# Performance work log

Measured on AMD Instinct MI355X. Metric: run time of the kernel, lower is better.

The kernel has to match this reference:

```python
import jax, jax.numpy as jnp
import numpy as np

N = 20000   # nodes
E = 160000  # edges
C = 512     # input_size / channels
D = 16      # edge_size
H = 256     # hidden_size
EPS = 1e-5  # BatchNorm eps (eval mode, init running stats: mean=0, var=1)


def setup_inputs() -> dict:
    key = jax.random.key(0)
    ks = jax.random.split(key, 24)
    w = lambda k, shape: (jax.random.normal(k, shape, jnp.float32) * 0.02)
    inp = {
        "x": jax.random.normal(ks[0], (N, C), jnp.float32),
        "edge_index": jax.random.randint(ks[1], (2, E), 0, N, jnp.int32),
        "edge_attr": jax.random.normal(ks[2], (E, D), jnp.float32),
        "goal_feat": jax.random.normal(ks[3], (N, C), jnp.float32),
        # CGConv 1
        "Wf1": w(ks[4], (2 * C + D, C)), "bf1": jnp.zeros((C,), jnp.float32),
        "Ws1": w(ks[5], (2 * C + D, C)), "bs1": jnp.zeros((C,), jnp.float32),
        "g1": jnp.ones((C,), jnp.float32), "be1": jnp.zeros((C,), jnp.float32),
        # CGConv 2
        "Wf2": w(ks[6], (2 * C + D, C)), "bf2": jnp.zeros((C,), jnp.float32),
        "Ws2": w(ks[7], (2 * C + D, C)), "bs2": jnp.zeros((C,), jnp.float32),
        "g2": jnp.ones((C,), jnp.float32), "be2": jnp.zeros((C,), jnp.float32),
        # GCNConv 3, 4
        "W3": w(ks[8], (C, H)), "b3": jnp.zeros((H,), jnp.float32),
        "W4": w(ks[9], (H, H)), "b4": jnp.zeros((H,), jnp.float32),
        # distance MLP: Lin(H+C -> C), ReLU, Lin(C -> 1)
        "Wd1": w(ks[10], (H + C, C)), "bd1": jnp.zeros((C,), jnp.float32),
        "Wd2": w(ks[11], (C, 1)), "bd2": jnp.zeros((1,), jnp.float32),
    }
    return inp


def cg_conv(x, src, dst, edge_attr, Wf, bf, Ws, bs, gamma, beta):
    # PyG CGConv: z = x_i || x_j || e;  m = sigmoid(lin_f(z)) * softplus(lin_s(z))
    # aggr='add' at targets, BatchNorm (eval, init stats), residual.
    z = jnp.concatenate([x[dst], x[src], edge_attr], axis=-1)  # [E, 2C+D]
    m = jax.nn.sigmoid(z @ Wf + bf) * jax.nn.softplus(z @ Ws + bs)  # [E, C]
    agg = jax.ops.segment_sum(m, dst, num_segments=N)  # [N, C]
    agg = agg * (gamma / jnp.sqrt(1.0 + EPS)) + beta   # BN eval (mean=0, var=1)
    return agg + x


def gcn_conv(x, src, dst, W, b):
    # PyG GCNConv with add_self_loops=True, normalize=True
    h = x @ W  # [N, out]
    loop = jnp.arange(N, dtype=src.dtype)
    s = jnp.concatenate([src, loop])
    d = jnp.concatenate([dst, loop])
    deg = jax.ops.segment_sum(jnp.ones_like(d, jnp.float32), d, num_segments=N)
    dinv = jnp.where(deg > 0, jax.lax.rsqrt(jnp.maximum(deg, 1.0)), 0.0)
    norm = dinv[s] * dinv[d]  # [E+N]
    out = jax.ops.segment_sum(norm[:, None] * h[s], d, num_segments=N)
    return out + b


def reference(x, edge_index, edge_attr, goal_feat,
              Wf1, bf1, Ws1, bs1, g1, be1,
              Wf2, bf2, Ws2, bs2, g2, be2,
              W3, b3, W4, b4, Wd1, bd1, Wd2, bd2):
    src = edge_index[0]  # x_j (source)
    dst = edge_index[1]  # x_i (target)
    h = jax.nn.relu(cg_conv(x, src, dst, edge_attr, Wf1, bf1, Ws1, bs1, g1, be1))
    h = jax.nn.relu(cg_conv(h, src, dst, edge_attr, Wf2, bf2, Ws2, bs2, g2, be2))
    h = jax.nn.relu(gcn_conv(h, src, dst, W3, b3))
    h = jax.nn.relu(gcn_conv(h, src, dst, W4, b4))
    z = jnp.concatenate([h, goal_feat], axis=1)  # [N, H+C]
    pred_dist = jax.nn.relu(z @ Wd1 + bd1) @ Wd2 + bd2  # [N, 1]
    return pred_dist, h
```

## Files before the change

### kernel.cpp

```cpp
#include <hip/hip_runtime.h>
#include <stdint.h>

#define NNODES 20000
#define NEDGES 160000
#define NPAD   20096

typedef float f32x4 __attribute__((ext_vector_type(4)));
typedef float f32x2 __attribute__((ext_vector_type(2)));
typedef short s16x8 __attribute__((ext_vector_type(8)));
typedef unsigned int u32x4 __attribute__((ext_vector_type(4)));
typedef _Float16 h16x2 __attribute__((ext_vector_type(2)));

#define L2E 1.44269504088896340736f
#define LN2 0.6931471805599453f

__device__ __forceinline__ float b2f(unsigned short b) {
    unsigned int u = ((unsigned int)b) << 16;
    return __builtin_bit_cast(float, u);
}
__device__ __forceinline__ unsigned short f2b(float f) {
    unsigned int u = __builtin_bit_cast(unsigned int, f);
    unsigned int r = (u + 0x7FFFu + ((u >> 16) & 1u)) >> 16;
    return (unsigned short)r;
}
__device__ __forceinline__ f32x2 unpack2(unsigned int u) {
    f32x2 r;
    r.x = __builtin_bit_cast(float, u << 16);
    r.y = __builtin_bit_cast(float, u & 0xFFFF0000u);
    return r;
}
__device__ __forceinline__ unsigned int packh2(float a, float b) {
    h16x2 h = { (_Float16)a, (_Float16)b };
    return __builtin_bit_cast(unsigned int, h);
}
__device__ __forceinline__ float dot2h(unsigned int a, unsigned int b, float c) {
#if __has_builtin(__builtin_amdgcn_fdot2)
    return __builtin_amdgcn_fdot2(__builtin_bit_cast(h16x2, a),
                                  __builtin_bit_cast(h16x2, b), c, false);
#else
    float d;
    asm("v_dot2_f32_f16 %0, %1, %2, %3" : "=v"(d) : "v"(a), "v"(b), "v"(c));
    return d;
#endif
}
__device__ __forceinline__ float exp2f_fast(float x) {
#if __has_builtin(__builtin_amdgcn_exp2f)
    return __builtin_amdgcn_exp2f(x);
#else
    return __builtin_exp2f(x);
#endif
}
__device__ __forceinline__ float log2f_fast(float x) {
#if __has_builtin(__builtin_amdgcn_logf)
    return __builtin_amdgcn_logf(x);
#else
    return __builtin_log2f(x);
#endif
}

__global__ __launch_bounds__(256) void gemm_bt_kernel(
    const unsigned short* __restrict__ A,
    const unsigned short* __restrict__ BT,
    float* __restrict__ Cf,
    unsigned short* __restrict__ Cb,
    int M, int N, int K,
    const float* __restrict__ bias)
{
    __shared__ unsigned short As[128 * 64];
    __shared__ unsigned short Bs[128 * 64];
    const int tid  = threadIdx.x;
    const int wid  = tid >> 6;
    const int lane = tid & 63;

    const int nwg  = gridDim.x * gridDim.y;
    const int orig = blockIdx.y * gridDim.x + blockIdx.x;
    const int q = nwg >> 3, r = nwg & 7;
    const int xcd = orig & 7;
    const int idx = orig >> 3;
    const int swz = (xcd < r ? xcd * (q + 1) : r * (q + 1) + (xcd - r) * q) + idx;
    const int bm = (swz / gridDim.y) * 128;
    const int bn = (swz % gridDim.y) * 128;

    const int wm = (wid & 1) * 64;
    const int wn = (wid >> 1) * 64;

    f32x4 acc[4][4];
#pragma unroll
    for (int i = 0; i < 4; i++)
#pragma unroll
        for (int j = 0; j < 4; j++) acc[i][j] = {0.f, 0.f, 0.f, 0.f};

    for (int k0 = 0; k0 < K; k0 += 64) {
#pragma unroll
        for (int rr = 0; rr < 4; rr++) {
            int flat = rr * 256 + tid;
            int row  = flat >> 3;
            int part = flat & 7;
            int pg   = part ^ (row & 7);
            const unsigned short* ga = A  + (size_t)(bm + row) * K + k0 + pg * 8;
            const unsigned short* gb = BT + (size_t)(bn + row) * K + k0 + pg * 8;
            __builtin_amdgcn_global_load_lds(
                (const __attribute__((address_space(1))) unsigned int*)ga,
                (__attribute__((address_space(3))) unsigned int*)&As[flat * 8], 16, 0, 0);
            __builtin_amdgcn_global_load_lds(
                (const __attribute__((address_space(1))) unsigned int*)gb,
                (__attribute__((address_space(3))) unsigned int*)&Bs[flat * 8], 16, 0, 0);
        }
        __syncthreads();

        const int kq8 = lane >> 4;
        const int rl  = lane & 15;
#pragma unroll
        for (int kk = 0; kk < 2; kk++) {
            s16x8 af[4], bfr[4];
#pragma unroll
            for (int mi = 0; mi < 4; mi++) {
                int row = wm + mi * 16 + rl;
                int slot = (kk * 4 + kq8) ^ (row & 7);
                af[mi] = *(const s16x8*)&As[row * 64 + slot * 8];
            }
#pragma unroll
            for (int ni = 0; ni < 4; ni++) {
                int row = wn + ni * 16 + rl;
                int slot = (kk * 4 + kq8) ^ (row & 7);
                bfr[ni] = *(const s16x8*)&Bs[row * 64 + slot * 8];
            }
#pragma unroll
            for (int mi = 0; mi < 4; mi++)
#pragma unroll
                for (int ni = 0; ni < 4; ni++)
                    acc[mi][ni] = __builtin_amdgcn_mfma_f32_16x16x32_bf16(
                        af[mi], bfr[ni], acc[mi][ni], 0, 0, 0);
        }
        __syncthreads();
    }

    const int cl = lane & 15;
    const int rq = (lane >> 4) * 4;
#pragma unroll
    for (int mi = 0; mi < 4; mi++)
#pragma unroll
        for (int ni = 0; ni < 4; ni++)
#pragma unroll
            for (int rr = 0; rr < 4; rr++) {
                int row = bm + wm + mi * 16 + rq + rr;
                int col = bn + wn + ni * 16 + cl;
                float v = acc[mi][ni][rr];
                if (Cb) {
                    if (bias) v = fmaxf(v + bias[col], 0.f);
                    Cb[(size_t)row * N + col] = f2b(v);
                } else {
                    Cf[(size_t)row * N + col] = v;
                }
            }
}

__global__ void count_kernel(const int* __restrict__ ei, int* __restrict__ counts) {
    int e = blockIdx.x * blockDim.x + threadIdx.x;
    if (e < NEDGES) atomicAdd(&counts[ei[NEDGES + e]], 1);
}

__global__ __launch_bounds__(1024) void scan_kernel(const int* __restrict__ counts,
                                                    int* __restrict__ row_ptr)
{
    __shared__ int sdata[1024];
    const int t = threadIdx.x;
    int vals[20];
    const int base = t * 20;
    int lsum = 0;
#pragma unroll
    for (int j = 0; j < 20; j++) {
        int idx = base + j;
        int v = (idx < NNODES) ? counts[idx] : 0;
        vals[j] = v; lsum += v;
    }
    sdata[t] = lsum;
    __syncthreads();
    for (int off = 1; off < 1024; off <<= 1) {
        int v = (t >= off) ? sdata[t - off] : 0;
        __syncthreads();
        sdata[t] += v;
        __syncthreads();
    }
    int run = sdata[t] - lsum;
#pragma unroll
    for (int j = 0; j < 20; j++) {
        int idx = base + j;
        if (idx < NNODES) row_ptr[idx] = run;
        run += vals[j];
    }
    if (t == 1023) row_ptr[NNODES] = sdata[1023];
}

__global__ void fill_kernel(const int* __restrict__ ei,
                            const int* __restrict__ row_ptr,
                            int* __restrict__ cursor,
                            int* __restrict__ csr_src,
                            int* __restrict__ csr_eid)
{
    int e = blockIdx.x * blockDim.x + threadIdx.x;
    if (e >= NEDGES) return;
    int dst = ei[NEDGES + e];
    int p = row_ptr[dst] + atomicAdd(&cursor[dst], 1);
    csr_src[p] = ei[e];
    csr_eid[p] = e;
}

__global__ void dinv_kernel(const int* __restrict__ row_ptr, float* __restrict__ dinv) {
    int i = blockIdx.x * blockDim.x + threadIdx.x;
    if (i < NNODES) {
        int deg = row_ptr[i + 1] - row_ptr[i] + 1;
        dinv[i] = rsqrtf((float)deg);
    }
}

__global__ void pad_copy_kernel(const float* __restrict__ src,
                                unsigned short* __restrict__ dst,
                                int valid_rows, int cols, long total)
{
    long idx = (long)blockIdx.x * blockDim.x + threadIdx.x;
    if (idx >= total) return;
    int n = (int)(idx / cols);
    dst[idx] = (n < valid_rows) ? f2b(src[idx]) : (unsigned short)0;
}

__global__ __launch_bounds__(256) void pack_cgw_kernel(
    const float* __restrict__ Wf,
    const float* __restrict__ Ws,
    unsigned short* __restrict__ out)
{
    __shared__ float tile[64][65];
    const int tx  = threadIdx.x & 63;
    const int ty4 = threadIdx.x >> 6;
    const int c0 = blockIdx.x * 64;
    const int k0 = blockIdx.y * 64;
    const int fs   = blockIdx.z & 1;
    const int half = blockIdx.z >> 1;
    const float* W = fs ? Ws : Wf;
    const float* Wb = W + (size_t)(half ? 512 : 0) * 512;
    for (int rr = ty4; rr < 64; rr += 4)
        tile[rr][tx] = Wb[(size_t)(k0 + rr) * 512 + (c0 + tx)];
    __syncthreads();
    for (int rr = ty4; rr < 64; rr += 4) {
        int c = c0 + rr;
        int j = half * 1024 + (c >> 1) * 4 + fs * 2 + (c & 1);
        out[(size_t)j * 512 + (k0 + tx)] = f2b(tile[tx][rr] * L2E);
    }
}

__global__ __launch_bounds__(256) void pack_t_kernel(
    const float* __restrict__ W,
    unsigned short* __restrict__ WT,
    int K, int Nout)
{
    __shared__ float tile[64][65];
    const int tx  = threadIdx.x & 63;
    const int ty4 = threadIdx.x >> 6;
    const int j0 = blockIdx.x * 64;
    const int k0 = blockIdx.y * 64;
    for (int rr = ty4; rr < 64; rr += 4)
        tile[rr][tx] = W[(size_t)(k0 + rr) * Nout + (j0 + tx)];
    __syncthreads();
    for (int rr = ty4; rr < 64; rr += 4)
        WT[(size_t)(j0 + rr) * K + (k0 + tx)] = f2b(tile[tx][rr]);
}

__global__ void pack_we_kernel(const float* __restrict__ Wf,
                               const float* __restrict__ Ws,
                               unsigned int* __restrict__ out)
{
    int idx = blockIdx.x * blockDim.x + threadIdx.x;
    if (idx >= 8192) return;
    int tid = idx >> 5;
    int r   = idx & 31;
    int k   = r >> 2;
    int q   = r & 3;
    const float* W = (q >> 1) ? Ws : Wf;
    int c = tid * 2 + (q & 1);
    float v0 = W[(size_t)(1024 + 2 * k) * 512 + c] * L2E;
    float v1 = W[(size_t)(1024 + 2 * k + 1) * 512 + c] * L2E;
    out[idx] = packh2(v0, v1);
}

__global__ void pack_ea_kernel(const int* __restrict__ csr_eid,
                               const float* __restrict__ ea,
                               unsigned int* __restrict__ out)
{
    int idx = blockIdx.x * blockDim.x + threadIdx.x;
    if (idx >= NEDGES * 8) return;
    int i = idx >> 3;
    int j = idx & 7;
    int eid = csr_eid[i];
    out[idx] = packh2(ea[(size_t)eid * 16 + 2 * j], ea[(size_t)eid * 16 + 2 * j + 1]);
}

#define CG_NPB 4

#define CG_LOADE(q_, a0_, a1_, jj) do {                                        \
    int sx_ = __builtin_amdgcn_readlane(sxv, (jj));                            \
    q_  = *(const uint2*)(P + (size_t)sx_ * 2048 + 1024 + c0 * 2);             \
    a0_ = eapk[(size_t)(base + (jj)) * 2];                                     \
    a1_ = eapk[(size_t)(base + (jj)) * 2 + 1];                                 \
} while (0)

#define CG_COMP(q_, a0_, a1_) do {                                             \
    float f0 = baseF.x, f1 = baseF.y, s0 = baseS.x, s1 = baseS.y;              \
    f0 = dot2h(a0_[0], w0[0], f0); f1 = dot2h(a0_[0], w0[1], f1);              \
    s0 = dot2h(a0_[0], w0[2], s0); s1 = dot2h(a0_[0], w0[3], s1);              \
    f0 = dot2h(a0_[1], w1[0], f0); f1 = dot2h(a0_[1], w1[1], f1);              \
    s0 = dot2h(a0_[1], w1[2], s0); s1 = dot2h(a0_[1], w1[3], s1);              \
    f0 = dot2h(a0_[2], w2[0], f0); f1 = dot2h(a0_[2], w2[1], f1);              \
    s0 = dot2h(a0_[2], w2[2], s0); s1 = dot2h(a0_[2], w2[3], s1);              \
    f0 = dot2h(a0_[3], w3[0], f0); f1 = dot2h(a0_[3], w3[1], f1);              \
    s0 = dot2h(a0_[3], w3[2], s0); s1 = dot2h(a0_[3], w3[3], s1);              \
    f0 = dot2h(a1_[0], w4[0], f0); f1 = dot2h(a1_[0], w4[1], f1);              \
    s0 = dot2h(a1_[0], w4[2], s0); s1 = dot2h(a1_[0], w4[3], s1);              \
    f0 = dot2h(a1_[1], w5[0], f0); f1 = dot2h(a1_[1], w5[1], f1);              \
    s0 = dot2h(a1_[1], w5[2], s0); s1 = dot2h(a1_[1], w5[3], s1);              \
    f0 = dot2h(a1_[2], w6[0], f0); f1 = dot2h(a1_[2], w6[1], f1);              \
    s0 = dot2h(a1_[2], w6[2], s0); s1 = dot2h(a1_[2], w6[3], s1);              \
    f0 = dot2h(a1_[3], w7[0], f0); f1 = dot2h(a1_[3], w7[1], f1);              \
    s0 = dot2h(a1_[3], w7[2], s0); s1 = dot2h(a1_[3], w7[3], s1);              \
    f32x2 pf = unpack2(q_.x);                                                  \
    f32x2 ps = unpack2(q_.y);                                                  \
    f0 += pf.x; f1 += pf.y; s0 += ps.x; s1 += ps.y;                            \
    float sp0 = log2f_fast(1.f + exp2f_fast(s0));                              \
    float sp1 = log2f_fast(1.f + exp2f_fast(s1));                              \
    float sg0 = __builtin_amdgcn_rcpf(1.f + exp2f_fast(-f0));                  \
    float sg1 = __builtin_amdgcn_rcpf(1.f + exp2f_fast(-f1));                  \
    acc.x = fmaf(sp0, sg0, acc.x);                                             \
    acc.y = fmaf(sp1, sg1, acc.y);                                             \
} while (0)

__global__ __launch_bounds__(256, 1) void cg_gather_kernel(
    const unsigned short* __restrict__ P,
    const int* __restrict__ row_ptr,
    const int* __restrict__ csr_src,
    const unsigned int* __restrict__ wE,
    const u32x4* __restrict__ eapk,
    const float* __restrict__ bfv,
    const float* __restrict__ bsv,
    const float* __restrict__ g,
    const float* __restrict__ be,
    const float* __restrict__ xresf,
    const unsigned short* __restrict__ xresb,
    unsigned short* __restrict__ hout)
{
    const int tid  = threadIdx.x;
    const int lane = tid & 63;
    const int c0  = tid * 2;
    const int nbase = blockIdx.x * CG_NPB;

    const unsigned int* wp = wE + (size_t)tid * 32;
    u32x4 w0, w1, w2, w3, w4, w5, w6, w7;
    asm volatile(
        "global_load_dwordx4 %0, %8, off\n\t"
        "global_load_dwordx4 %1, %8, off offset:16\n\t"
        "global_load_dwordx4 %2, %8, off offset:32\n\t"
        "global_load_dwordx4 %3, %8, off offset:48\n\t"
        "global_load_dwordx4 %4, %8, off offset:64\n\t"
        "global_load_dwordx4 %5, %8, off offset:80\n\t"
        "global_load_dwordx4 %6, %8, off offset:96\n\t"
        "global_load_dwordx4 %7, %8, off offset:112\n\t"
        "s_waitcnt vmcnt(0)"
        : "=&v"(w0), "=&v"(w1), "=&v"(w2), "=&v"(w3),
          "=&v"(w4), "=&v"(w5), "=&v"(w6), "=&v"(w7)
        : "v"(wp));
    __builtin_amdgcn_sched_barrier(0);

    const f32x2 bfx = *(const f32x2*)&bfv[c0] * L2E;
    const f32x2 bsx = *(const f32x2*)&bsv[c0] * L2E;
    const f32x2 gv  = *(const f32x2*)&g[c0];
    const f32x2 bev = *(const f32x2*)&be[c0];
    const float rsl = rsqrtf(1.f + 1e-5f) * LN2;

    for (int n = nbase; n < nbase + CG_NPB; n++) {
        if (n >= NNODES) {
            *(unsigned int*)&hout[(size_t)n * 512 + c0] = 0;
            continue;
        }
        const unsigned short* Pd = P + (size_t)n * 2048;
        const uint2 qb = *(const uint2*)(Pd + c0 * 2);
        const f32x2 baseF = unpack2(qb.x) + bfx;
        const f32x2 baseS = unpack2(qb.y) + bsx;

        f32x2 acc = {0.f, 0.f};
        const int i0 = __builtin_amdgcn_readfirstlane(row_ptr[n]);
        const int i1 = __builtin_amdgcn_readfirstlane(row_ptr[n + 1]);

        for (int base = i0; base < i1; base += 64) {
            const int cnt = min(64, i1 - base);
            int idxc = base + lane;
            if (idxc >= NEDGES) idxc = NEDGES - 1;
            const int sxv = csr_src[idxc];

            uint2 qA = {}, qB = {};
            u32x4 aA0 = {}, aA1 = {}, aB0 = {}, aB1 = {};
            CG_LOADE(qA, aA0, aA1, 0);
            if (cnt > 1) CG_LOADE(qB, aB0, aB1, 1);
            int j = 0;
            while (true) {
                CG_COMP(qA, aA0, aA1);
                if (j + 2 < cnt) CG_LOADE(qA, aA0, aA1, j + 2);
                if (++j >= cnt) break;
                CG_COMP(qB, aB0, aB1);
                if (j + 2 < cnt) CG_LOADE(qB, aB0, aB1, j + 2);
                if (++j >= cnt) break;
            }
        }

        f32x2 res;
        if (xresf) {
            res = *(const f32x2*)&xresf[(size_t)n * 512 + c0];
        } else {
            res = unpack2(*(const unsigned int*)&xresb[(size_t)n * 512 + c0]);
        }
        float v0 = fmaxf(acc.x * (gv.x * rsl) + bev.x + res.x, 0.f);
        float v1 = fmaxf(acc.y * (gv.y * rsl) + bev.y + res.y, 0.f);
        unsigned int packed = (unsigned int)f2b(v0) | ((unsigned int)f2b(v1) << 16);
        *(unsigned int*)&hout[(size_t)n * 512 + c0] = packed;
    }
}

__global__ __launch_bounds__(256) void gcn_gather_kernel(
    const unsigned short* __restrict__ pre,
    const int* __restrict__ row_ptr,
    const int* __restrict__ csr_src,
    const float* __restrict__ dinv,
    const float* __restrict__ b,
    unsigned short* __restrict__ hout,
    float* __restrict__ doutf)
{
    const int tid  = threadIdx.x;
    const int lane = tid & 63;
    const int n = blockIdx.x * 4 + (tid >> 6);
    const int c = lane * 4;
    if (n >= NNODES) {
        if (n < NPAD) { uint2 z = {0u, 0u}; *(uint2*)&hout[(size_t)n * 256 + c] = z; }
        return;
    }
    const float din = dinv[n];
    f32x4 acc = {0.f, 0.f, 0.f, 0.f};
    const int i0 = __builtin_amdgcn_readfirstlane(row_ptr[n]);
    const int i1 = __builtin_amdgcn_readfirstlane(row_ptr[n + 1]);

#define GCN_LD(pv_, jj) do {                                                   \
    int sx_ = __builtin_amdgcn_readlane(sxv, (jj));                            \
    pv_ = *(const uint2*)&pre[(size_t)sx_ * 256 + c];                          \
} while (0)

#define GCN_CP(pv_, jj) do {                                                   \
    float dv_ = __builtin_bit_cast(float, __builtin_amdgcn_readlane(dvb, (jj)));\
    f32x2 p0 = unpack2(pv_.x);                                                 \
    f32x2 p1 = unpack2(pv_.y);                                                 \
    acc.x = fmaf(dv_, p0.x, acc.x);                                            \
    acc.y = fmaf(dv_, p0.y, acc.y);                                            \
    acc.z = fmaf(dv_, p1.x, acc.z);                                            \
    acc.w = fmaf(dv_, p1.y, acc.w);                                            \
} while (0)

    for (int base = i0; base < i1; base += 64) {
        const int cnt = min(64, i1 - base);
        int idxc = base + lane;
        if (idxc >= NEDGES) idxc = NEDGES - 1;
        const int sxv = csr_src[idxc];
        const int dvb = __builtin_bit_cast(int, dinv[sxv]);

        uint2 pvA = {}, pvB = {}, pvC = {};
        GCN_LD(pvA, 0);
        if (cnt > 1) GCN_LD(pvB, 1);
        if (cnt > 2) GCN_LD(pvC, 2);
        int j = 0;
        while (true) {
            GCN_CP(pvA, j);
            if (j + 3 < cnt) GCN_LD(pvA, j + 3);
            if (++j >= cnt) break;
            GCN_CP(pvB, j);
            if (j + 3 < cnt) GCN_LD(pvB, j + 3);
            if (++j >= cnt) break;
            GCN_CP(pvC, j);
            if (j + 3 < cnt) GCN_LD(pvC, j + 3);
            if (++j >= cnt) break;
        }
    }
    uint2 sv = *(const uint2*)&pre[(size_t)n * 256 + c];
    f32x2 s0 = unpack2(sv.x);
    f32x2 s1 = unpack2(sv.y);
    const f32x4 bv = *(const f32x4*)&b[c];
    const float d2 = din * din;
    float v0 = fmaxf(fmaf(acc.x, din, d2 * s0.x) + bv.x, 0.f);
    float v1 = fmaxf(fmaf(acc.y, din, d2 * s0.y) + bv.y, 0.f);
    float v2 = fmaxf(fmaf(acc.z, din, d2 * s1.x) + bv.z, 0.f);
    float v3 = fmaxf(fmaf(acc.w, din, d2 * s1.y) + bv.w, 0.f);
    uint2 o;
    o.x = (unsigned int)f2b(v0) | ((unsigned int)f2b(v1) << 16);
    o.y = (unsigned int)f2b(v2) | ((unsigned int)f2b(v3) << 16);
    *(uint2*)&hout[(size_t)n * 256 + c] = o;
    if (doutf) {
        f32x4 vv = {v0, v1, v2, v3};
        *(f32x4*)&doutf[(size_t)n * 256 + c] = vv;
    }
}

__global__ void build_zc_kernel(const unsigned short* __restrict__ h4,
                                const float* __restrict__ goal,
                                unsigned short* __restrict__ zc)
{
    long idx = (long)blockIdx.x * blockDim.x + threadIdx.x;
    if (idx >= (long)NPAD * 768) return;
    int n = (int)(idx / 768);
    int c = (int)(idx % 768);
    unsigned short v = 0;
    if (n < NNODES)
        v = (c < 256) ? h4[(size_t)n * 256 + c]
                      : f2b(goal[(size_t)n * 512 + (c - 256)]);
    zc[idx] = v;
}

__global__ __launch_bounds__(256) void final_dot_kernel(
    const unsigned short* __restrict__ t,
    const float* __restrict__ Wd2,
    const float* __restrict__ bd2,
    float* __restrict__ pred)
{
    const int lane = threadIdx.x & 63;
    const int wid  = threadIdx.x >> 6;
    float w[8];
#pragma unroll
    for (int i = 0; i < 8; i++) w[i] = Wd2[lane * 8 + i];
    const float bd = bd2[0];
    for (int n = blockIdx.x * 4 + wid; n < NNODES; n += gridDim.x * 4) {
        const unsigned short* tp = t + (size_t)n * 512 + lane * 8;
        float s = 0.f;
#pragma unroll
        for (int i = 0; i < 8; i++) s = fmaf(b2f(tp[i]), w[i], s);
#pragma unroll
        for (int off = 32; off; off >>= 1) s += __shfl_xor(s, off, 64);
        if (lane == 0) pred[n] = s + bd;
    }
}

extern "C" void kernel_launch(void* const* d_in, const int* in_sizes, int n_in,
                              void* d_out, int out_size, void* d_ws, size_t ws_size,
                              hipStream_t stream)
{
    (void)in_sizes; (void)n_in; (void)out_size; (void)ws_size;
    const float* x    = (const float*)d_in[0];
    const int*   ei   = (const int*)d_in[1];
    const float* ea   = (const float*)d_in[2];
    const float* goal = (const float*)d_in[3];
    const float* Wf1  = (const float*)d_in[4];
    const float* bf1  = (const float*)d_in[5];
    const float* Ws1  = (const float*)d_in[6];
    const float* bs1  = (const float*)d_in[7];
    const float* g1   = (const float*)d_in[8];
    const float* be1  = (const float*)d_in[9];
    const float* Wf2  = (const float*)d_in[10];
    const float* bf2  = (const float*)d_in[11];
    const float* Ws2  = (const float*)d_in[12];
    const float* bs2  = (const float*)d_in[13];
    const float* g2   = (const float*)d_in[14];
    const float* be2  = (const float*)d_in[15];
    const float* W3   = (const float*)d_in[16];
    const float* b3   = (const float*)d_in[17];
    const float* W4   = (const float*)d_in[18];
    const float* b4   = (const float*)d_in[19];
    const float* Wd1  = (const float*)d_in[20];
    const float* bd1  = (const float*)d_in[21];
    const float* Wd2  = (const float*)d_in[22];
    const float* bd2  = (const float*)d_in[23];
    float* outp = (float*)d_out;

    char* ws = (char*)d_ws;
    size_t off = 0;
    auto alloc = [&](size_t bytes) -> char* {
        char* p = ws + off;
        off += (bytes + 255) & ~(size_t)255;
        return p;
    };
    unsigned short* P     = (unsigned short*)alloc((size_t)NPAD * 2048 * 2);
    unsigned short* bufA  = (unsigned short*)alloc((size_t)NPAD * 512 * 2);
    unsigned short* bufB  = (unsigned short*)alloc((size_t)NPAD * 512 * 2);
    unsigned short* bufC  = (unsigned short*)alloc((size_t)NPAD * 512 * 2);
    unsigned short* wpack = (unsigned short*)alloc((size_t)2048 * 512 * 2);
    int*            counts  = (int*)alloc((size_t)NNODES * 4);
    int*            row_ptr = (int*)alloc((size_t)(NNODES + 1) * 4);
    int*            csr_src = (int*)alloc((size_t)NEDGES * 4);
    int*            csr_eid = (int*)alloc((size_t)NEDGES * 4);
    float*          dinv    = (float*)alloc((size_t)NNODES * 4);
    unsigned int*   wEbuf   = (unsigned int*)alloc((size_t)8192 * 4);
    unsigned int*   eapk    = (unsigned int*)alloc((size_t)NEDGES * 8 * 4);

    unsigned short* xpad  = bufA;
    unsigned short* h1    = bufB;
    unsigned short* h2    = bufA;
    unsigned short* pre_b = bufB;
    unsigned short* h3    = bufC;
    unsigned short* h4    = bufA;
    unsigned short* zc    = P;
    unsigned short* tb    = P + (size_t)NPAD * 1024;

    const int B = 256;

    hipMemsetAsync(counts, 0, (size_t)NNODES * 4, stream);
    count_kernel<<<(NEDGES + B - 1) / B, B, 0, stream>>>(ei, counts);
    scan_kernel<<<1, 1024, 0, stream>>>(counts, row_ptr);
    hipMemsetAsync(counts, 0, (size_t)NNODES * 4, stream);
    fill_kernel<<<(NEDGES + B - 1) / B, B, 0, stream>>>(ei, row_ptr, counts, csr_src, csr_eid);
    dinv_kernel<<<(NNODES + B - 1) / B, B, 0, stream>>>(row_ptr, dinv);
    pack_ea_kernel<<<(NEDGES * 8 + B - 1) / B, B, 0, stream>>>(csr_eid, ea, eapk);

    {
        long tot = (long)NPAD * 512;
        pad_copy_kernel<<<(unsigned)((tot + B - 1) / B), B, 0, stream>>>(x, xpad, NNODES, 512, tot);
    }

    dim3 gBig(NPAD / 128, 2048 / 128);

    pack_cgw_kernel<<<dim3(8, 8, 4), B, 0, stream>>>(Wf1, Ws1, wpack);
    pack_we_kernel<<<(8192 + B - 1) / B, B, 0, stream>>>(Wf1, Ws1, wEbuf);
    gemm_bt_kernel<<<gBig, B, 0, stream>>>(xpad, wpack, nullptr, P, NPAD, 2048, 512, nullptr);
    cg_gather_kernel<<<NPAD / CG_NPB, B, 0, stream>>>(P, row_ptr, csr_src,
                                                      wEbuf, (const u32x4*)eapk,
                                                      bf1, bs1, g1, be1,
                                                      x, nullptr, h1);

    pack_cgw_kernel<<<dim3(8, 8, 4), B, 0, stream>>>(Wf2, Ws2, wpack);
    gemm_bt_kernel<<<gBig, B, 0, stream>>>(h1, wpack, nullptr, P, NPAD, 2048, 512, nullptr);
    pack_we_kernel<<<(8192 + B - 1) / B, B, 0, stream>>>(Wf2, Ws2, wEbuf);
    cg_gather_kernel<<<NPAD / CG_NPB, B, 0, stream>>>(P, row_ptr, csr_src,
                                                      wEbuf, (const u32x4*)eapk,
                                                      bf2, bs2, g2, be2,
                                                      nullptr, h1, h2);

    pack_t_kernel<<<dim3(256 / 64, 512 / 64), B, 0, stream>>>(W3, wpack, 512, 256);
    gemm_bt_kernel<<<dim3(NPAD / 128, 2), B, 0, stream>>>(h2, wpack, nullptr, pre_b, NPAD, 256, 512, nullptr);
    gcn_gather_kernel<<<NPAD / 4, B, 0, stream>>>(pre_b, row_ptr, csr_src, dinv, b3, h3, (float*)nullptr);

    pack_t_kernel<<<dim3(256 / 64, 256 / 64), B, 0, stream>>>(W4, wpack, 256, 256);
    gemm_bt_kernel<<<dim3(NPAD / 128, 2), B, 0, stream>>>(h3, wpack, nullptr, pre_b, NPAD, 256, 256, nullptr);
    gcn_gather_kernel<<<NPAD / 4, B, 0, stream>>>(pre_b, row_ptr, csr_src, dinv, b4, h4, outp + NNODES);

    build_zc_kernel<<<(unsigned)(((long)NPAD * 768 + B - 1) / B), B, 0, stream>>>(h4, goal, zc);
    pack_t_kernel<<<dim3(512 / 64, 768 / 64), B, 0, stream>>>(Wd1, wpack, 768, 512);
    gemm_bt_kernel<<<dim3(NPAD / 128, 4), B, 0, stream>>>(zc, wpack, nullptr, tb, NPAD, 512, 768, bd1);
    final_dot_kernel<<<512, B, 0, stream>>>(tb, Wd2, bd2, outp);
}
```

Measured before the change: 751.8 us.

## Flatten CG gather edge loop across nodes and vectorize padding copies

```diff
diff --git a/kernel.cpp b/kernel.cpp
--- a/kernel.cpp
+++ b/kernel.cpp
@@ -216,12 +216,23 @@
 
 __global__ void pad_copy_kernel(const float* __restrict__ src,
                                 unsigned short* __restrict__ dst,
-                                int valid_rows, int cols, long total)
+                                long total8)
 {
     long idx = (long)blockIdx.x * blockDim.x + threadIdx.x;
-    if (idx >= total) return;
-    int n = (int)(idx / cols);
-    dst[idx] = (n < valid_rows) ? f2b(src[idx]) : (unsigned short)0;
+    if (idx >= total8) return;
+    int n  = (int)(idx >> 6);
+    int c8 = ((int)idx & 63) * 8;
+    uint4 o = {0u, 0u, 0u, 0u};
+    if (n < NNODES) {
+        const float* sp = src + (size_t)n * 512 + c8;
+        f32x4 a = *(const f32x4*)sp;
+        f32x4 b = *(const f32x4*)(sp + 4);
+        o.x = (unsigned)f2b(a.x) | ((unsigned)f2b(a.y) << 16);
+        o.y = (unsigned)f2b(a.z) | ((unsigned)f2b(a.w) << 16);
+        o.z = (unsigned)f2b(b.x) | ((unsigned)f2b(b.y) << 16);
+        o.w = (unsigned)f2b(b.z) | ((unsigned)f2b(b.w) << 16);
+    }
+    *(uint4*)&dst[(size_t)n * 512 + c8] = o;
 }
 
 __global__ __launch_bounds__(256) void pack_cgw_kernel(
@@ -294,7 +305,7 @@
     out[idx] = packh2(ea[(size_t)eid * 16 + 2 * j], ea[(size_t)eid * 16 + 2 * j + 1]);
 }
 
-#define CG_NPB 4
+#define CG_NPB 8
 
 #define CG_LOADE(q_, a0_, a1_, jj) do {                                        \
     int sx_ = __builtin_amdgcn_readlane(sxv, (jj));                            \
@@ -332,6 +343,24 @@
     acc.y = fmaf(sp1, sg1, acc.y);                                             \
 } while (0)
 
+#define CG_FINAL() do {                                                        \
+    int nn_ = nbase + cur;                                                     \
+    unsigned int packed_ = 0u;                                                 \
+    if (nn_ < NNODES) {                                                        \
+        float v0_ = fmaxf(acc.x * (gv.x * rsl) + bev.x + resC.x, 0.f);         \
+        float v1_ = fmaxf(acc.y * (gv.y * rsl) + bev.y + resC.y, 0.f);         \
+        packed_ = (unsigned int)f2b(v0_) | ((unsigned int)f2b(v1_) << 16);     \
+    }                                                                          \
+    *(unsigned int*)&hout[(size_t)nn_ * 512 + c0] = packed_;                   \
+    cur++;                                                                     \
+    qbC = qbN; resC = resN;                                                    \
+    if (cur + 1 < CG_NPB) { qbN = loadQB(cur + 1); resN = loadRes(cur + 1); }  \
+    baseF = unpack2(qbC.x) + bfx;                                              \
+    baseS = unpack2(qbC.y) + bsx;                                              \
+    acc.x = 0.f; acc.y = 0.f;                                                  \
+    bnd = __builtin_amdgcn_readlane(rpl, cur + 1 < CG_NPB ? cur + 1 : CG_NPB); \
+} while (0)
+
 __global__ __launch_bounds__(256, 1) void cg_gather_kernel(
     const unsigned short* __restrict__ P,
     const int* __restrict__ row_ptr,
@@ -374,52 +403,58 @@
     const f32x2 bev = *(const f32x2*)&be[c0];
     const float rsl = rsqrtf(1.f + 1e-5f) * LN2;
 
-    for (int n = nbase; n < nbase + CG_NPB; n++) {
-        if (n >= NNODES) {
-            *(unsigned int*)&hout[(size_t)n * 512 + c0] = 0;
-            continue;
+    int rpidx = nbase + (lane < CG_NPB ? lane : CG_NPB);
+    if (rpidx > NNODES) rpidx = NNODES;
+    const int rpl = row_ptr[rpidx];
+    const int e0 = __builtin_amdgcn_readlane(rpl, 0);
+    const int e1 = __builtin_amdgcn_readlane(rpl, CG_NPB);
+
+    auto loadQB = [&](int s) -> uint2 {
+        int nn = nbase + s;
+        if (nn >= NNODES) { uint2 z = {0u, 0u}; return z; }
+        return *(const uint2*)(P + (size_t)nn * 2048 + c0 * 2);
+    };
+    auto loadRes = [&](int s) -> f32x2 {
+        int nn = nbase + s;
+        f32x2 z = {0.f, 0.f};
+        if (nn >= NNODES) return z;
+        if (xresf) return *(const f32x2*)&xresf[(size_t)nn * 512 + c0];
+        return unpack2(*(const unsigned int*)&xresb[(size_t)nn * 512 + c0]);
+    };
+
+    int cur = 0;
+    uint2 qbC = loadQB(0);
+    f32x2 resC = loadRes(0);
+    uint2 qbN = loadQB(1);
+    f32x2 resN = loadRes(1);
+    f32x2 baseF = unpack2(qbC.x) + bfx;
+    f32x2 baseS = unpack2(qbC.y) + bsx;
+    f32x2 acc = {0.f, 0.f};
+    int bnd = __builtin_amdgcn_readlane(rpl, 1);
+
+    for (int base = e0; base < e1; base += 64) {
+        const int cnt = min(64, e1 - base);
+        int idxc = base + lane;
+        if (idxc >= NEDGES) idxc = NEDGES - 1;
+        const int sxv = csr_src[idxc];
+
+        uint2 qA = {}, qB = {};
+        u32x4 aA0 = {}, aA1 = {}, aB0 = {}, aB1 = {};
+        CG_LOADE(qA, aA0, aA1, 0);
+        if (cnt > 1) CG_LOADE(qB, aB0, aB1, 1);
+        int j = 0;
+        while (true) {
+            while (base + j >= bnd) CG_FINAL();
+            CG_COMP(qA, aA0, aA1);
+            if (j + 2 < cnt) CG_LOADE(qA, aA0, aA1, j + 2);
+            if (++j >= cnt) break;
+            while (base + j >= bnd) CG_FINAL();
+            CG_COMP(qB, aB0, aB1);
+            if (j + 2 < cnt) CG_LOADE(qB, aB0, aB1, j + 2);
+            if (++j >= cnt) break;
         }
-        const unsigned short* Pd = P + (size_t)n * 2048;
-        const uint2 qb = *(const uint2*)(Pd + c0 * 2);
-        const f32x2 baseF = unpack2(qb.x) + bfx;
-        const f32x2 baseS = unpack2(qb.y) + bsx;
-
-        f32x2 acc = {0.f, 0.f};
-        const int i0 = __builtin_amdgcn_readfirstlane(row_ptr[n]);
-        const int i1 = __builtin_amdgcn_readfirstlane(row_ptr[n + 1]);
-
-        for (int base = i0; base < i1; base += 64) {
-            const int cnt = min(64, i1 - base);
-            int idxc = base + lane;
-            if (idxc >= NEDGES) idxc = NEDGES - 1;
-            const int sxv = csr_src[idxc];
-
-            uint2 qA = {}, qB = {};
-            u32x4 aA0 = {}, aA1 = {}, aB0 = {}, aB1 = {};
-            CG_LOADE(qA, aA0, aA1, 0);
-            if (cnt > 1) CG_LOADE(qB, aB0, aB1, 1);
-            int j = 0;
-            while (true) {
-                CG_COMP(qA, aA0, aA1);
-                if (j + 2 < cnt) CG_LOADE(qA, aA0, aA1, j + 2);
-                if (++j >= cnt) break;
-                CG_COMP(qB, aB0, aB1);
-                if (j + 2 < cnt) CG_LOADE(qB, aB0, aB1, j + 2);
-                if (++j >= cnt) break;
-            }
-        }
-
-        f32x2 res;
-        if (xresf) {
-            res = *(const f32x2*)&xresf[(size_t)n * 512 + c0];
-        } else {
-            res = unpack2(*(const unsigned int*)&xresb[(size_t)n * 512 + c0]);
-        }
-        float v0 = fmaxf(acc.x * (gv.x * rsl) + bev.x + res.x, 0.f);
-        float v1 = fmaxf(acc.y * (gv.y * rsl) + bev.y + res.y, 0.f);
-        unsigned int packed = (unsigned int)f2b(v0) | ((unsigned int)f2b(v1) << 16);
-        *(unsigned int*)&hout[(size_t)n * 512 + c0] = packed;
-    }
+    }
+    while (cur < CG_NPB) CG_FINAL();
 }
 
 __global__ __launch_bounds__(256) void gcn_gather_kernel(
@@ -502,19 +537,36 @@
     }
 }
 
-__global__ void build_zc_kernel(const unsigned short* __restrict__ h4,
-                                const float* __restrict__ goal,
-                                unsigned short* __restrict__ zc)
-{
-    long idx = (long)blockIdx.x * blockDim.x + threadIdx.x;
-    if (idx >= (long)NPAD * 768) return;
-    int n = (int)(idx / 768);
-    int c = (int)(idx % 768);
-    unsigned short v = 0;
-    if (n < NNODES)
-        v = (c < 256) ? h4[(size_t)n * 256 + c]
-                      : f2b(goal[(size_t)n * 512 + (c - 256)]);
-    zc[idx] = v;
+__global__ void zc_h4_kernel(const unsigned short* __restrict__ h4,
+                             unsigned short* __restrict__ zc)
+{
+    int idx = blockIdx.x * blockDim.x + threadIdx.x;
+    if (idx >= NPAD * 32) return;
+    int n  = idx >> 5;
+    int c8 = (idx & 31) * 8;
+    uint4 v = {0u, 0u, 0u, 0u};
+    if (n < NNODES) v = *(const uint4*)&h4[(size_t)n * 256 + c8];
+    *(uint4*)&zc[(size_t)n * 768 + c8] = v;
+}
+
+__global__ void zc_goal_kernel(const float* __restrict__ goal,
+                               unsigned short* __restrict__ zc)
+{
+    int idx = blockIdx.x * blockDim.x + threadIdx.x;
+    if (idx >= NPAD * 64) return;
+    int n  = idx >> 6;
+    int c8 = (idx & 63) * 8;
+    uint4 o = {0u, 0u, 0u, 0u};
+    if (n < NNODES) {
+        const float* sp = goal + (size_t)n * 512 + c8;
+        f32x4 a = *(const f32x4*)sp;
+        f32x4 b = *(const f32x4*)(sp + 4);
+        o.x = (unsigned)f2b(a.x) | ((unsigned)f2b(a.y) << 16);
+        o.y = (unsigned)f2b(a.z) | ((unsigned)f2b(a.w) << 16);
+        o.z = (unsigned)f2b(b.x) | ((unsigned)f2b(b.y) << 16);
+        o.w = (unsigned)f2b(b.z) | ((unsigned)f2b(b.w) << 16);
+    }
+    *(uint4*)&zc[(size_t)n * 768 + 256 + c8] = o;
 }
 
 __global__ __launch_bounds__(256) void final_dot_kernel(
@@ -611,8 +663,8 @@
     pack_ea_kernel<<<(NEDGES * 8 + B - 1) / B, B, 0, stream>>>(csr_eid, ea, eapk);
 
     {
-        long tot = (long)NPAD * 512;
-        pad_copy_kernel<<<(unsigned)((tot + B - 1) / B), B, 0, stream>>>(x, xpad, NNODES, 512, tot);
+        long tot8 = (long)NPAD * 64;
+        pad_copy_kernel<<<(unsigned)((tot8 + B - 1) / B), B, 0, stream>>>(x, xpad, tot8);
     }
 
     dim3 gBig(NPAD / 128, 2048 / 128);
@@ -641,7 +693,8 @@
     gemm_bt_kernel<<<dim3(NPAD / 128, 2), B, 0, stream>>>(h3, wpack, nullptr, pre_b, NPAD, 256, 256, nullptr);
     gcn_gather_kernel<<<NPAD / 4, B, 0, stream>>>(pre_b, row_ptr, csr_src, dinv, b4, h4, outp + NNODES);
 
-    build_zc_kernel<<<(unsigned)(((long)NPAD * 768 + B - 1) / B), B, 0, stream>>>(h4, goal, zc);
+    zc_h4_kernel<<<(NPAD * 32 + B - 1) / B, B, 0, stream>>>(h4, zc);
+    zc_goal_kernel<<<(NPAD * 64 + B - 1) / B, B, 0, stream>>>(goal, zc);
     pack_t_kernel<<<dim3(512 / 64, 768 / 64), B, 0, stream>>>(Wd1, wpack, 768, 512);
     gemm_bt_kernel<<<dim3(NPAD / 128, 4), B, 0, stream>>>(zc, wpack, nullptr, tb, NPAD, 512, 768, bd1);
     final_dot_kernel<<<512, B, 0, stream>>>(tb, Wd2, bd2, outp);
```

After: 730.9 us. 1.03x faster.
